# Kernel optimization log

Hardware: AMD Instinct MI355X
Metric: run time of the kernel (lower is better)

## Reference

```python
import jax, jax.numpy as jnp
import numpy as np

B = 4; C = 3; IMG = 256; P = 16; HP = 16; HW = 256
DIM = 512; DEPTH = 6; HEADS = 8; DH = 64
NS = 50; SH = 4; SDH = 64; ITERS = 3; RPD = 128; FF = 2048; N = NS + HW


def _ln(x, g, b):
    m = jnp.mean(x, -1, keepdims=True)
    v = jnp.var(x, -1, keepdims=True)
    return (x - m) * jax.lax.rsqrt(v + 1e-5) * g + b


def _rms(x, g):
    # lucidrains RMSNorm: F.normalize(x, dim=-1) * sqrt(dim) * gamma
    n = jnp.linalg.norm(x, axis=-1, keepdims=True)
    return x / jnp.maximum(n, 1e-12) * (DIM ** 0.5) * g


def setup_inputs() -> dict:
    key = jax.random.key(0)
    ks = iter(jax.random.split(key, 64))
    def W(*s):
        return jax.random.normal(next(ks), s, jnp.float32) * 0.02
    SI = SH * SDH
    d = {}
    d['images'] = jax.random.normal(next(ks), (B, C, IMG, IMG), jnp.float32)
    d['slot_noise'] = jax.random.normal(next(ks), (B, NS, DIM), jnp.float32)
    d['patch_w'] = W(C * P * P, DIM); d['patch_b'] = jnp.zeros((DIM,))
    d['hpos'] = W(HP, DIM); d['wpos'] = W(HP, DIM)
    d['rp_w1'] = W(2, RPD); d['rp_b1'] = jnp.zeros((RPD,))
    d['rp_w2'] = W(RPD, RPD); d['rp_b2'] = jnp.zeros((RPD,))
    d['rp_w3'] = W(RPD, HEADS); d['rp_b3'] = jnp.zeros((HEADS,))
    d['slots_mu'] = W(1, 1, DIM); d['slots_logsigma'] = jnp.zeros((1, 1, DIM))
    d['sa_ln_in_g'] = jnp.ones((DIM,)); d['sa_ln_in_b'] = jnp.zeros((DIM,))
    d['sa_ln_sl_g'] = jnp.ones((DIM,)); d['sa_ln_sl_b'] = jnp.zeros((DIM,))
    d['sa_wq'] = W(DIM, SI); d['sa_bq'] = jnp.zeros((SI,))
    d['sa_wk'] = W(DIM, SI); d['sa_bk'] = jnp.zeros((SI,))
    d['sa_wv'] = W(DIM, SI); d['sa_bv'] = jnp.zeros((SI,))
    d['sa_wo'] = W(SI, DIM); d['sa_bo'] = jnp.zeros((DIM,))
    d['gru_wih'] = W(DIM, 3 * DIM); d['gru_whh'] = W(DIM, 3 * DIM)
    d['gru_bih'] = jnp.zeros((3 * DIM,)); d['gru_bhh'] = jnp.zeros((3 * DIM,))
    d['sa_ln_ff_g'] = jnp.ones((DIM,)); d['sa_ln_ff_b'] = jnp.zeros((DIM,))
    d['sa_mlp_w1'] = W(DIM, DIM); d['sa_mlp_b1'] = jnp.zeros((DIM,))
    d['sa_mlp_w2'] = W(DIM, DIM); d['sa_mlp_b2'] = jnp.zeros((DIM,))
    d['s2c_w'] = W(DIM, 2); d['s2c_b'] = jnp.zeros((2,))
    d['attn_g'] = jnp.ones((DEPTH, DIM))
    d['wq'] = W(DEPTH, DIM, HEADS * DH); d['wk'] = W(DEPTH, DIM, HEADS * DH)
    d['wv'] = W(DEPTH, DIM, HEADS * DH); d['wo'] = W(DEPTH, HEADS * DH, DIM)
    d['ff_g'] = jnp.ones((DEPTH, DIM))
    d['ff_w1'] = W(DEPTH, DIM, FF); d['ff_b1'] = jnp.zeros((DEPTH, FF))
    d['ff_w2'] = W(DEPTH, FF, DIM); d['ff_b2'] = jnp.zeros((DEPTH, DIM))
    d['final_g'] = jnp.ones((DIM,))
    d['pred_w'] = W(DIM, DIM); d['pred_b'] = jnp.zeros((DIM,))
    return d


def reference(images, slot_noise, patch_w, patch_b, hpos, wpos,
              rp_w1, rp_b1, rp_w2, rp_b2, rp_w3, rp_b3,
              slots_mu, slots_logsigma, sa_ln_in_g, sa_ln_in_b, sa_ln_sl_g, sa_ln_sl_b,
              sa_wq, sa_bq, sa_wk, sa_bk, sa_wv, sa_bv, sa_wo, sa_bo,
              gru_wih, gru_whh, gru_bih, gru_bhh, sa_ln_ff_g, sa_ln_ff_b,
              sa_mlp_w1, sa_mlp_b1, sa_mlp_w2, sa_mlp_b2, s2c_w, s2c_b,
              attn_g, wq, wk, wv, wo, ff_g, ff_w1, ff_b1, ff_w2, ff_b2,
              final_g, pred_w, pred_b):
    b = images.shape[0]
    # patchify: b c (h p1) (w p2) -> b h w (p1 p2 c)
    x = images.reshape(b, C, HP, P, HP, P).transpose(0, 2, 4, 3, 5, 1).reshape(b, HP, HP, P * P * C)
    tokens = x @ patch_w + patch_b                     # [b, HP, HP, DIM]
    tokens = tokens + hpos[:, None, :] + wpos[None, :, :]
    tokens = tokens.reshape(b, HW, DIM)
    # --- multi-head slot attention ---
    inp = _ln(tokens, sa_ln_in_g, sa_ln_in_b)
    k = (inp @ sa_wk + sa_bk).reshape(b, HW, SH, SDH).transpose(0, 2, 1, 3)
    v = (inp @ sa_wv + sa_bv).reshape(b, HW, SH, SDH).transpose(0, 2, 1, 3)
    slots = slots_mu + jnp.exp(slots_logsigma) * slot_noise  # [b, NS, DIM]
    scale = SDH ** -0.5
    for _ in range(ITERS):
        prev = slots
        s = _ln(slots, sa_ln_sl_g, sa_ln_sl_b)
        q = (s @ sa_wq + sa_bq).reshape(b, NS, SH, SDH).transpose(0, 2, 1, 3)
        dots = jnp.einsum('bhid,bhjd->bhij', q, k) * scale     # [b, SH, NS, HW]
        attn = jax.nn.softmax(dots, axis=-2) + 1e-8            # softmax over slots
        attn = attn / jnp.sum(attn, -1, keepdims=True)         # weighted mean over inputs
        upd = jnp.einsum('bhij,bhjd->bhid', attn, v)
        upd = upd.transpose(0, 2, 1, 3).reshape(b, NS, SH * SDH) @ sa_wo + sa_bo
        # GRUCell(updates, prev_slots)
        gx = upd @ gru_wih + gru_bih
        gh = prev @ gru_whh + gru_bhh
        xr, xz, xn = jnp.split(gx, 3, -1)
        hr, hz, hn = jnp.split(gh, 3, -1)
        r = jax.nn.sigmoid(xr + hr)
        z = jax.nn.sigmoid(xz + hz)
        nn_ = jnp.tanh(xn + r * hn)
        slots = (1 - z) * nn_ + z * prev
        slots = slots + (jax.nn.relu(_ln(slots, sa_ln_ff_g, sa_ln_ff_b) @ sa_mlp_w1 + sa_mlp_b1) @ sa_mlp_w2 + sa_mlp_b2)
    objects = slots
    slot_coords = objects @ s2c_w + s2c_b              # [b, NS, 2]
    # --- relative position MLP bias (slots coords + patch grid) ---
    g = jnp.arange(HP, dtype=jnp.float32)
    grid = jnp.stack(jnp.meshgrid(g, g, indexing='ij'), -1).reshape(HW, 2)
    coords = jnp.concatenate([slot_coords, jnp.broadcast_to(grid, (b, HW, 2))], axis=1)  # [b, N, 2]
    rel = coords[:, :, None, :] - coords[:, None, :, :]   # [b, N, N, 2]
    hmid = jax.nn.silu(rel @ rp_w1 + rp_b1)
    hmid = jax.nn.silu(hmid @ rp_w2 + rp_b2)
    bias = jnp.transpose(hmid @ rp_w3 + rp_b3, (0, 3, 1, 2))  # [b, HEADS, N, N]
    # --- transformer with per-layer rel-pos bias ---
    x = jnp.concatenate([objects, tokens], axis=1)     # [b, N, DIM]
    ascale = DH ** -0.5
    for l in range(DEPTH):
        h = _rms(x, attn_g[l])
        qh = (h @ wq[l]).reshape(b, N, HEADS, DH).transpose(0, 2, 1, 3)
        kh = (h @ wk[l]).reshape(b, N, HEADS, DH).transpose(0, 2, 1, 3)
        vh = (h @ wv[l]).reshape(b, N, HEADS, DH).transpose(0, 2, 1, 3)
        sim = jnp.einsum('bhid,bhjd->bhij', qh, kh) * ascale + bias
        a = jax.nn.softmax(sim, -1)
        o = jnp.einsum('bhij,bhjd->bhid', a, vh).transpose(0, 2, 1, 3).reshape(b, N, HEADS * DH) @ wo[l]
        x = x + o
        h = _rms(x, ff_g[l])
        x = x + (jax.nn.gelu(h @ ff_w1[l] + ff_b1[l]) @ ff_w2[l] + ff_b2[l])
    x = _rms(x, final_g)
    return x[:, NS:] @ pred_w + pred_b                 # [b, HW, DIM]
```

## Files before the change

### kernel.cpp

```cpp
#include <hip/hip_runtime.h>
#include <hip/hip_bf16.h>

typedef __hip_bfloat16 bf16;
typedef short short8v __attribute__((ext_vector_type(8)));
typedef float float4v __attribute__((ext_vector_type(4)));

static __device__ __forceinline__ float b2f(bf16 x){ return __bfloat162float(x); }

static __device__ __forceinline__ float ldin(const void* p, size_t i, bool isbf) {
  return isbf ? b2f(((const bf16*)p)[i]) : ((const float*)p)[i];
}

static __device__ __forceinline__ unsigned short f2bu(float f) {
  bf16 h = __float2bfloat16(f);
  return *reinterpret_cast<unsigned short*>(&h);
}

#define CDIV(a,b) (((a)+(b)-1)/(b))

#define NB   4
#define NSL  50
#define HWT  256
#define NT   306
#define DIM  512
#define NH   8
#define FF   2048
#define RPP  28100
#define PCH  56200

static __device__ __forceinline__ void rp_decode(int q, int& i, int& j) {
  if (q < 15300) { i = q / NT; j = q % NT; }
  else { int r = q - 15300; i = NSL + r / NSL; j = r % NSL; }
}

__global__ void detect_k(const void* p, int* flag) {
  const unsigned short* u = (const unsigned short*)p;
  int t = threadIdx.x;
  int e = (u[t] >> 7) & 0xFF;
  __shared__ int anybad;
  if (t == 0) anybad = 0;
  __syncthreads();
  if (e >= 0x88) atomicOr(&anybad, 1);
  __syncthreads();
  if (t == 0) *flag = anybad ? 0 : 1;
}

struct WtArgs {
  const void* W[17];
  unsigned long long wto[17];
  int K[17], N[17];
  int base[18];
};

__global__ __launch_bounds__(256) void wtrans_all_k(WtArgs a, unsigned short* __restrict__ WT,
                                                    const int* __restrict__ flagp) {
  const bool isbf = *flagp != 0;
  int bid = blockIdx.x;
  int idx = 0;
#pragma unroll
  for (int i = 1; i < 17; ++i) if (bid >= a.base[i]) idx = i;
  int t0 = bid - a.base[idx];
  const int K = a.K[idx], N = a.N[idx];
  const int tilesN = N >> 6;
  const int perLayer = tilesN * (K >> 6);
  const int layer = t0 / perLayer, rem = t0 % perLayer;
  const int n0 = (rem % tilesN) * 64, k0 = (rem / tilesN) * 64;
  const void* W = a.W[idx];
  unsigned short* dst0 = WT + a.wto[idx];
  const size_t slice = (size_t)K * N * layer;

  __shared__ unsigned short S[64 * 72];
  int t = threadIdx.x;
  int kk = t >> 4, nn = (t & 15) * 4;
#pragma unroll
  for (int r = 0; r < 4; ++r) {
    int k = k0 + kk + r * 16;
    unsigned short v[4];
    if (isbf) {
      ushort4 u = *(const ushort4*)((const unsigned short*)W + slice + (size_t)k * N + n0 + nn);
      v[0]=u.x; v[1]=u.y; v[2]=u.z; v[3]=u.w;
    } else {
      float4 f = *(const float4*)((const float*)W + slice + (size_t)k * N + n0 + nn);
      v[0]=f2bu(f.x); v[1]=f2bu(f.y); v[2]=f2bu(f.z); v[3]=f2bu(f.w);
    }
#pragma unroll
    for (int i = 0; i < 4; ++i) S[(nn + i) * 72 + kk + r * 16] = v[i];
  }
  __syncthreads();
  int nr = t >> 2, kc = (t & 3) * 16;
  short8v s0 = *(const short8v*)&S[nr * 72 + kc];
  short8v s1 = *(const short8v*)&S[nr * 72 + kc + 8];
  unsigned short* dst = dst0 + slice + (size_t)(n0 + nr) * K + k0 + kc;
  *(short8v*)dst = s0;
  *(short8v*)(dst + 8) = s1;
}

#define LDK 72
static __device__ __forceinline__ void gemm_body2(
    const void* __restrict__ A, int aty,
    const unsigned short* __restrict__ WT,
    const void* __restrict__ bias, size_t boff,
    void* __restrict__ C, int oty,
    int M, int N, int K, int kbeg, int kend,
    int act, int mode, bool isbf)
{
  __shared__ unsigned short As[64 * LDK];
  __shared__ unsigned short Bs[64 * LDK];
  const int tid = threadIdx.x;
  const int lane = tid & 63, wave = tid >> 6;
  const int quad = lane >> 4, ti = lane & 15;
  const int wm = (wave & 1) * 32, wn = (wave >> 1) * 32;
  const int bm = blockIdx.y * 64, bn = blockIdx.x * 64;
  const int srow = tid >> 2, sch = (tid & 3) * 16;

  unsigned short ha[16], hb[16];
  const int gm = bm + srow;
  const bool aok = gm < M;
  const unsigned short* Abf = (const unsigned short*)A + (size_t)gm * K;
  const float*          Af  = (const float*)A + (size_t)gm * K;
  const unsigned short* Bp  = WT + (size_t)(bn + srow) * K;

  auto fetchA = [&](int k0) {
    if (aok) {
      if (aty) {
        const ushort4* ap = (const ushort4*)(Abf + k0 + sch);
#pragma unroll
        for (int i = 0; i < 4; ++i) {
          ushort4 u = ap[i];
          ha[i*4+0]=u.x; ha[i*4+1]=u.y; ha[i*4+2]=u.z; ha[i*4+3]=u.w;
        }
      } else {
        const float4* ap = (const float4*)(Af + k0 + sch);
#pragma unroll
        for (int i = 0; i < 4; ++i) {
          float4 f = ap[i];
          ha[i*4+0]=f2bu(f.x); ha[i*4+1]=f2bu(f.y); ha[i*4+2]=f2bu(f.z); ha[i*4+3]=f2bu(f.w);
        }
      }
    } else {
#pragma unroll
      for (int i = 0; i < 16; ++i) ha[i] = 0;
    }
  };
  auto fetchB = [&](int k0) {
    const ushort4* bp = (const ushort4*)(Bp + k0 + sch);
#pragma unroll
    for (int i = 0; i < 4; ++i) {
      ushort4 u = bp[i];
      hb[i*4+0]=u.x; hb[i*4+1]=u.y; hb[i*4+2]=u.z; hb[i*4+3]=u.w;
    }
  };

  float4v acc00 = {0,0,0,0}, acc01 = {0,0,0,0}, acc10 = {0,0,0,0}, acc11 = {0,0,0,0};
  fetchA(kbeg); fetchB(kbeg);
  for (int k0 = kbeg; k0 < kend; k0 += 64) {
    *(short8v*)&As[srow * LDK + sch]     = *(short8v*)ha;
    *(short8v*)&As[srow * LDK + sch + 8] = *(short8v*)(ha + 8);
    *(short8v*)&Bs[srow * LDK + sch]     = *(short8v*)hb;
    *(short8v*)&Bs[srow * LDK + sch + 8] = *(short8v*)(hb + 8);
    __syncthreads();
    if (k0 + 64 < kend) { fetchA(k0 + 64); fetchB(k0 + 64); }
#pragma unroll
    for (int ks = 0; ks < 2; ++ks) {
      short8v a0 = *reinterpret_cast<const short8v*>(&As[(wm + ti)      * LDK + ks * 32 + quad * 8]);
      short8v a1 = *reinterpret_cast<const short8v*>(&As[(wm + 16 + ti) * LDK + ks * 32 + quad * 8]);
      short8v b0 = *reinterpret_cast<const short8v*>(&Bs[(wn + ti)      * LDK + ks * 32 + quad * 8]);
      short8v b1 = *reinterpret_cast<const short8v*>(&Bs[(wn + 16 + ti) * LDK + ks * 32 + quad * 8]);
      acc00 = __builtin_amdgcn_mfma_f32_16x16x32_bf16(a0, b0, acc00, 0, 0, 0);
      acc01 = __builtin_amdgcn_mfma_f32_16x16x32_bf16(a0, b1, acc01, 0, 0, 0);
      acc10 = __builtin_amdgcn_mfma_f32_16x16x32_bf16(a1, b0, acc10, 0, 0, 0);
      acc11 = __builtin_amdgcn_mfma_f32_16x16x32_bf16(a1, b1, acc11, 0, 0, 0);
    }
    __syncthreads();
  }

  float4v accs[2][2] = {{acc00, acc01}, {acc10, acc11}};
#pragma unroll
  for (int mi = 0; mi < 2; ++mi) {
#pragma unroll
    for (int ni = 0; ni < 2; ++ni) {
      int row0 = bm + wm + mi * 16 + quad * 4;
      int col  = bn + wn + ni * 16 + ti;
      float bv = (bias && kbeg == 0) ? ldin(bias, boff + col, isbf) : 0.f;
#pragma unroll
      for (int r = 0; r < 4; ++r) {
        int row = row0 + r;
        if (row >= M) continue;
        float v = accs[mi][ni][r] + bv;
        if (act == 1) v = fmaxf(v, 0.f);
        else if (act == 2) {
          float u = 0.7978845608028654f * (v + 0.044715f * v * v * v);
          v = 0.5f * v * (1.f + tanhf(u));
        } else if (act == 3) {
          v = v / (1.f + expf(-v));
        }
        size_t idx = (size_t)row * N + col;
        if (oty) ((bf16*)C)[idx] = __float2bfloat16(v);
        else {
          float* Cf = (float*)C;
          if (mode == 2) atomicAdd(&Cf[idx], v);
          else if (mode == 1) Cf[idx] += v;
          else Cf[idx] = v;
        }
      }
    }
  }
}

__global__ __launch_bounds__(256) void gemm_mfma(
    const void* A, int aty, const unsigned short* WT, size_t woff,
    const void* bias, size_t boff, void* C, int oty,
    int M, int N, int K, int act, int accum, int zsplit, const int* __restrict__ flagp)
{
  int ksz = K / zsplit;
  int kbeg = blockIdx.z * ksz;
  int mode = zsplit > 1 ? 2 : (accum ? 1 : 0);
  gemm_body2(A, aty, WT + woff, bias, boff, C, oty, M, N, K, kbeg, kbeg + ksz,
             act, mode, *flagp != 0);
}

__global__ __launch_bounds__(256) void gemm_mfma_tri(
    const void* A, int aty, const unsigned short* WT, size_t o0, size_t o1, size_t o2,
    void* C0, void* C1, void* C2, int oty, int M, int N, int K,
    const int* __restrict__ flagp)
{
  size_t o = blockIdx.z == 0 ? o0 : (blockIdx.z == 1 ? o1 : o2);
  void* C = blockIdx.z == 0 ? C0 : (blockIdx.z == 1 ? C1 : C2);
  gemm_body2(A, aty, WT + o, nullptr, 0, C, oty, M, N, K, 0, K, 0, 0, *flagp != 0);
}

__global__ __launch_bounds__(256) void gemm_mfma_duo(
    const void* A0, const void* A1, int aty, const unsigned short* WT, size_t o0, size_t o1,
    const void* bias0, const void* bias1, void* C0, void* C1, int oty,
    int M, int N, int K, const int* __restrict__ flagp)
{
  const void* A = blockIdx.z ? A1 : A0;
  size_t o = blockIdx.z ? o1 : o0;
  const void* bias = blockIdx.z ? bias1 : bias0;
  void* C = blockIdx.z ? C1 : C0;
  gemm_body2(A, aty, WT + o, bias, 0, C, oty, M, N, K, 0, K, 0, 0, *flagp != 0);
}

__global__ void s2c_k(const float* __restrict__ slots, const void* __restrict__ w,
                      const void* __restrict__ bv, float* __restrict__ sc,
                      const int* __restrict__ flagp) {
  const bool isbf = *flagp != 0;
  int row = blockIdx.x, t = threadIdx.x;
  const float* x = slots + (size_t)row * DIM;
  float v0 = x[t], v1 = x[t + 256];
  float a0 = v0 * ldin(w, 2 * t, isbf)     + v1 * ldin(w, 2 * (t + 256), isbf);
  float a1 = v0 * ldin(w, 2 * t + 1, isbf) + v1 * ldin(w, 2 * (t + 256) + 1, isbf);
  __shared__ float r0[256], r1[256];
  r0[t] = a0; r1[t] = a1;
  __syncthreads();
  for (int o = 128; o > 0; o >>= 1) {
    if (t < o) { r0[t] += r0[t + o]; r1[t] += r1[t + o]; }
    __syncthreads();
  }
  if (t == 0) {
    sc[row * 2]     = r0[0] + ldin(bv, 0, isbf);
    sc[row * 2 + 1] = r1[0] + ldin(bv, 1, isbf);
  }
}

__global__ void patchify_k(const void* __restrict__ img, unsigned short* __restrict__ xp,
                           const int* __restrict__ flagp) {
  const bool isbf = *flagp != 0;
  int i = blockIdx.x * 256 + threadIdx.x;
  if (i >= NB * HWT * 768) return;
  int col = i % 768, row = i / 768;
  int c = col % 3, p2 = (col / 3) & 15, p1 = col / 48;
  int w = row & 15, h = (row >> 4) & 15, b = row >> 8;
  xp[i] = f2bu(ldin(img, (((size_t)(b * 3 + c) * 256 + h * 16 + p1) * 256) + w * 16 + p2, isbf));
}

__global__ void addpos_k(float* __restrict__ tok, const void* __restrict__ hp,
                         const void* __restrict__ wp, const int* __restrict__ flagp) {
  const bool isbf = *flagp != 0;
  int i = blockIdx.x * 256 + threadIdx.x;
  if (i >= NB * HWT * DIM) return;
  int d = i & 511;
  int row = i >> 9;
  int w = row & 15, h = (row >> 4) & 15;
  tok[i] += ldin(hp, h * DIM + d, isbf) + ldin(wp, w * DIM + d, isbf);
}

__global__ void ln512_k(const float* __restrict__ X, const void* __restrict__ g,
                        const void* __restrict__ b, unsigned short* __restrict__ Y,
                        const int* __restrict__ flagp) {
  const bool isbf = *flagp != 0;
  int row = blockIdx.x, t = threadIdx.x;
  const float* x = X + (size_t)row * DIM;
  float v0 = x[t], v1 = x[t + 256];
  __shared__ float rs[256], rq[256];
  rs[t] = v0 + v1; rq[t] = v0 * v0 + v1 * v1;
  __syncthreads();
  for (int o = 128; o > 0; o >>= 1) {
    if (t < o) { rs[t] += rs[t + o]; rq[t] += rq[t + o]; }
    __syncthreads();
  }
  float mean = rs[0] * (1.f / 512.f);
  float var  = rq[0] * (1.f / 512.f) - mean * mean;
  float inv  = rsqrtf(var + 1e-5f);
  unsigned short* y = Y + (size_t)row * DIM;
  y[t]       = f2bu((v0 - mean) * inv * ldin(g, t, isbf)       + ldin(b, t, isbf));
  y[t + 256] = f2bu((v1 - mean) * inv * ldin(g, t + 256, isbf) + ldin(b, t + 256, isbf));
}

__global__ void rms512_k(const float* __restrict__ X, const void* __restrict__ g,
                         int goff, unsigned short* __restrict__ Y, const int* __restrict__ flagp) {
  const bool isbf = *flagp != 0;
  int row = blockIdx.x, t = threadIdx.x;
  const float* x = X + (size_t)row * DIM;
  float v0 = x[t], v1 = x[t + 256];
  __shared__ float rq[256];
  rq[t] = v0 * v0 + v1 * v1;
  __syncthreads();
  for (int o = 128; o > 0; o >>= 1) {
    if (t < o) rq[t] += rq[t + o];
    __syncthreads();
  }
  float nrm = sqrtf(rq[0]);
  float sc = 22.62741699796952f / fmaxf(nrm, 1e-12f);
  unsigned short* y = Y + (size_t)row * DIM;
  y[t]       = f2bu(v0 * sc * ldin(g, goff + t, isbf));
  y[t + 256] = f2bu(v1 * sc * ldin(g, goff + t + 256, isbf));
}

__global__ void slots_init_k(const void* __restrict__ mu, const void* __restrict__ ls,
                             const void* __restrict__ noise, float* __restrict__ slots,
                             const int* __restrict__ flagp) {
  const bool isbf = *flagp != 0;
  int i = blockIdx.x * 256 + threadIdx.x;
  if (i >= NB * NSL * DIM) return;
  int d = i & 511;
  slots[i] = ldin(mu, d, isbf) + expf(ldin(ls, d, isbf)) * ldin(noise, i, isbf);
}

__global__ void slot_dots_k(const float* __restrict__ q, const float* __restrict__ k,
                            float* __restrict__ dots) {
  int blk = blockIdx.x;
  int i = blk % 50, h = (blk / 50) & 3, b = blk / 200;
  int j = threadIdx.x;
  __shared__ float qs[64];
  if (threadIdx.x < 64) qs[threadIdx.x] = q[((size_t)(b * 50 + i)) * 256 + h * 64 + threadIdx.x];
  __syncthreads();
  const float* kr = k + ((size_t)(b * 256 + j)) * 256 + h * 64;
  float s = 0.f;
#pragma unroll 8
  for (int d = 0; d < 64; ++d) s = fmaf(qs[d], kr[d], s);
  dots[(((size_t)(b * 4 + h) * 50) + i) * 256 + j] = s * 0.125f;
}

__global__ void softmax_slots_k(float* __restrict__ dots) {
  int idx = blockIdx.x * 256 + threadIdx.x;
  if (idx >= 4096) return;
  int j = idx & 255, h = (idx >> 8) & 3, b = idx >> 10;
  float* base = dots + ((size_t)(b * 4 + h) * 50) * 256 + j;
  float m = -1e30f;
  for (int i = 0; i < 50; ++i) m = fmaxf(m, base[i * 256]);
  float s = 0.f;
  for (int i = 0; i < 50; ++i) { float e = expf(base[i * 256] - m); base[i * 256] = e; s += e; }
  float inv = 1.f / s;
  for (int i = 0; i < 50; ++i) base[i * 256] *= inv;
}

__global__ void renorm_attn_k(float* __restrict__ attn) {
  int t = threadIdx.x;
  float* row = attn + (size_t)blockIdx.x * 256;
  float v = row[t] + 1e-8f;
  __shared__ float rs[256];
  rs[t] = v;
  __syncthreads();
  for (int o = 128; o > 0; o >>= 1) {
    if (t < o) rs[t] += rs[t + o];
    __syncthreads();
  }
  row[t] = v / rs[0];
}

__global__ void slot_upd_k(const float* __restrict__ attn, const float* __restrict__ v,
                           float* __restrict__ upd) {
  int bi = blockIdx.x;
  int b = bi / 50, i = bi % 50;
  int t = threadIdx.x, h = t >> 6;
  const float* arow = attn + ((size_t)((b * 4 + h) * 50) + i) * 256;
  float s = 0.f;
  for (int j = 0; j < 256; ++j) s = fmaf(arow[j], v[((size_t)(b * 256 + j)) * 256 + t], s);
  upd[(size_t)bi * 256 + t] = s;
}

__global__ void gru_k(const float* __restrict__ gx, const float* __restrict__ gh,
                      float* __restrict__ slots) {
  int i = blockIdx.x * 256 + threadIdx.x;
  if (i >= NB * NSL * DIM) return;
  int row = i >> 9, d = i & 511;
  size_t b3 = (size_t)row * 1536;
  float xr = gx[b3 + d], xz = gx[b3 + 512 + d], xn = gx[b3 + 1024 + d];
  float hr = gh[b3 + d], hz = gh[b3 + 512 + d], hn = gh[b3 + 1024 + d];
  float r = 1.f / (1.f + expf(-(xr + hr)));
  float z = 1.f / (1.f + expf(-(xz + hz)));
  float n = tanhf(xn + r * hn);
  float prev = slots[i];
  slots[i] = (1.f - z) * n + z * prev;
}

__global__ void build_coords_k(const float* __restrict__ sc, float* __restrict__ coords) {
  int i = blockIdx.x * 256 + threadIdx.x;
  if (i >= NB * NT) return;
  int b = i / NT, n = i % NT;
  float cx, cy;
  if (n < NSL) { cx = sc[(b * NSL + n) * 2]; cy = sc[(b * NSL + n) * 2 + 1]; }
  else { int t = n - NSL; cx = (float)(t >> 4); cy = (float)(t & 15); }
  coords[i * 2] = cx; coords[i * 2 + 1] = cy;
}

__global__ void relpos_table_k(const void* w1, const void* b1, const void* w2,
                               const void* b2, const void* w3, const void* b3,
                               float* __restrict__ tab, const int* __restrict__ flagp) {
  const bool isbf = *flagp != 0;
  int blk = blockIdx.x;
  float r0 = (float)(blk / 31 - 15), r1 = (float)(blk % 31 - 15);
  int t = threadIdx.x;
  __shared__ float h1[128], h2[128];
  float a = fmaf(r0, ldin(w1, t, isbf), fmaf(r1, ldin(w1, 128 + t, isbf), ldin(b1, t, isbf)));
  h1[t] = a / (1.f + expf(-a));
  __syncthreads();
  float s = ldin(b2, t, isbf);
#pragma unroll 4
  for (int k = 0; k < 128; ++k) s = fmaf(h1[k], ldin(w2, k * 128 + t, isbf), s);
  h2[t] = s / (1.f + expf(-s));
  __syncthreads();
  if (t < 8) {
    float o = ldin(b3, t, isbf);
#pragma unroll 4
    for (int k = 0; k < 128; ++k) o = fmaf(h2[k], ldin(w3, k * 8 + t, isbf), o);
    tab[blk * 8 + t] = o;
  }
}

__global__ void bias_fill_k(const float* __restrict__ tab, float* __restrict__ bias) {
  int i = blockIdx.x * 256 + threadIdx.x;
  if (i >= NB * NH * HWT * HWT) return;
  int jj = i & 255, ii = (i >> 8) & 255, h = (i >> 16) & 7, b = i >> 19;
  int di = (ii >> 4) - (jj >> 4) + 15;
  int dj = (ii & 15) - (jj & 15) + 15;
  bias[(((size_t)(b * NH + h) * NT) + NSL + ii) * NT + NSL + jj] = tab[(di * 31 + dj) * 8 + h];
}

__global__ void rp_l1_k(const float* __restrict__ coords, const void* w1, const void* b1,
                        unsigned short* __restrict__ H, int pbase, int pcount,
                        const int* __restrict__ flagp) {
  const bool isbf = *flagp != 0;
  int idx = blockIdx.x * 256 + threadIdx.x;
  if (idx >= pcount * 128) return;
  int pl = idx >> 7, u = idx & 127;
  int p = pbase + pl;
  int q = p % RPP, bb = p / RPP;
  int ii, jj;
  rp_decode(q, ii, jj);
  float r0 = coords[(bb * NT + ii) * 2]     - coords[(bb * NT + jj) * 2];
  float r1 = coords[(bb * NT + ii) * 2 + 1] - coords[(bb * NT + jj) * 2 + 1];
  float a = fmaf(r0, ldin(w1, u, isbf), fmaf(r1, ldin(w1, 128 + u, isbf), ldin(b1, u, isbf)));
  H[(size_t)pl * 128 + u] = f2bu(a / (1.f + expf(-a)));
}

__global__ __launch_bounds__(256) void rp_l3_k(
    const unsigned short* __restrict__ H2, const void* w3, const void* b3,
    float* __restrict__ bias, int pbase, int pcount, const int* __restrict__ flagp) {
  const bool isbf = *flagp != 0;
  __shared__ float W3s[128 * 8];
  int t = threadIdx.x;
  for (int e = t; e < 1024; e += 256) W3s[e] = ldin(w3, e, isbf);
  __syncthreads();
  int pl = blockIdx.x * 32 + (t >> 3), hh = t & 7;
  if (pl >= pcount) return;
  int p = pbase + pl;
  int q = p % RPP, bb = p / RPP;
  int ii, jj;
  rp_decode(q, ii, jj);
  float s = ldin(b3, hh, isbf);
  const unsigned short* hrow = H2 + (size_t)pl * 128;
#pragma unroll 8
  for (int k = 0; k < 128; ++k) {
    bf16 hv = *reinterpret_cast<const bf16*>(&hrow[k]);
    s = fmaf(b2f(hv), W3s[k * 8 + hh], s);
  }
  bias[((size_t)(bb * NH + hh) * NT + ii) * NT + jj] = s;
}

__global__ void build_x_k(const float* __restrict__ slots, const float* __restrict__ tok,
                          float* __restrict__ x) {
  int i = blockIdx.x * 256 + threadIdx.x;
  if (i >= NB * NT * DIM) return;
  int d = i & 511, n = (i >> 9) % NT, b = i / (NT * DIM);
  x[i] = (n < NSL) ? slots[((size_t)(b * NSL + n)) * DIM + d]
                   : tok[((size_t)(b * HWT + (n - NSL))) * DIM + d];
}

__global__ __launch_bounds__(256) void attn_fused_k(
    const unsigned short* __restrict__ Qb, const unsigned short* __restrict__ Kb,
    const unsigned short* __restrict__ Vb, const float* __restrict__ bias,
    unsigned short* __restrict__ Ob)
{
  const int bh = blockIdx.y, b = bh >> 3, h = bh & 7;
  const int i0 = blockIdx.x * 32;
  __shared__ unsigned short Qs[32 * 72];
  __shared__ unsigned short Ks[64 * 72];
  __shared__ float S[32 * 332];
  unsigned short* P = (unsigned short*)S;

  const int tid = threadIdx.x;
  const int lane = tid & 63, wave = tid >> 6, quad = lane >> 4, ti = lane & 15;
  const int mi = wave & 1, nh = wave >> 1;

  {
    int r = tid >> 3, c = (tid & 7) * 8;
    int gi = i0 + r;
    ushort4 u0 = {0,0,0,0}, u1 = {0,0,0,0};
    if (gi < NT) {
      const ushort4* p = (const ushort4*)(Qb + ((size_t)(b * NT + gi)) * DIM + h * 64 + c);
      u0 = p[0]; u1 = p[1];
    }
    *(ushort4*)&Qs[r * 72 + c] = u0;
    *(ushort4*)&Qs[r * 72 + c + 4] = u1;
  }

  for (int kt = 0; kt < 5; ++kt) {
    __syncthreads();
    {
      int kr = tid >> 2, c = (tid & 3) * 16;
      int gj = kt * 64 + kr;
      ushort4 v[4] = {{0,0,0,0},{0,0,0,0},{0,0,0,0},{0,0,0,0}};
      if (gj < NT) {
        const ushort4* p = (const ushort4*)(Kb + ((size_t)(b * NT + gj)) * DIM + h * 64 + c);
#pragma unroll
        for (int i = 0; i < 4; ++i) v[i] = p[i];
      }
#pragma unroll
      for (int i = 0; i < 4; ++i) *(ushort4*)&Ks[kr * 72 + c + i * 4] = v[i];
    }
    __syncthreads();
#pragma unroll
    for (int ntl = 0; ntl < 2; ++ntl) {
      int nt = nh * 2 + ntl;
      float4v acc = {0,0,0,0};
#pragma unroll
      for (int ks = 0; ks < 2; ++ks) {
        short8v a  = *(const short8v*)&Qs[(mi * 16 + ti) * 72 + ks * 32 + quad * 8];
        short8v bb = *(const short8v*)&Ks[(nt * 16 + ti) * 72 + ks * 32 + quad * 8];
        acc = __builtin_amdgcn_mfma_f32_16x16x32_bf16(a, bb, acc, 0, 0, 0);
      }
      int colL = kt * 64 + nt * 16 + ti;
      int row0 = mi * 16 + quad * 4;
#pragma unroll
      for (int r = 0; r < 4; ++r) {
        int row_g = i0 + row0 + r;
        float val;
        if (colL < NT) {
          float bv = (row_g < NT) ? bias[((size_t)bh * NT + row_g) * NT + colL] : 0.f;
          val = acc[r] * 0.125f + bv;
        } else val = -1e30f;
        S[(row0 + r) * 332 + colL] = val;
      }
    }
  }
  __syncthreads();

  {
    int rl = tid >> 3, sub = tid & 7;
    float sv[40];
#pragma unroll
    for (int k = 0; k < 40; ++k) sv[k] = S[rl * 332 + sub + k * 8];
    float m = -1e30f;
#pragma unroll
    for (int k = 0; k < 40; ++k) m = fmaxf(m, sv[k]);
    m = fmaxf(m, __shfl_xor(m, 1));
    m = fmaxf(m, __shfl_xor(m, 2));
    m = fmaxf(m, __shfl_xor(m, 4));
    float s = 0.f;
#pragma unroll
    for (int k = 0; k < 40; ++k) { float e = __expf(sv[k] - m); sv[k] = e; s += e; }
    s += __shfl_xor(s, 1);
    s += __shfl_xor(s, 2);
    s += __shfl_xor(s, 4);
    float inv = 1.f / s;
    __syncthreads();
#pragma unroll
    for (int k = 0; k < 40; ++k) P[rl * 664 + sub + k * 8] = f2bu(sv[k] * inv);
  }

  float4v oacc[2] = {{0,0,0,0},{0,0,0,0}};
  for (int vt = 0; vt < 5; ++vt) {
    __syncthreads();
    {
      int key = tid & 63, d0 = (tid >> 6) * 16;
      int gj = vt * 64 + key;
      unsigned short hv[16];
      if (gj < NT) {
        const ushort4* p = (const ushort4*)(Vb + ((size_t)(b * NT + gj)) * DIM + h * 64 + d0);
#pragma unroll
        for (int i = 0; i < 4; ++i) {
          ushort4 u = p[i];
          hv[i*4+0]=u.x; hv[i*4+1]=u.y; hv[i*4+2]=u.z; hv[i*4+3]=u.w;
        }
      } else {
#pragma unroll
        for (int i = 0; i < 16; ++i) hv[i] = 0;
      }
#pragma unroll
      for (int i = 0; i < 16; ++i) Ks[(d0 + i) * 72 + key] = hv[i];
    }
    __syncthreads();
#pragma unroll
    for (int ntl = 0; ntl < 2; ++ntl) {
      int nt = nh * 2 + ntl;
#pragma unroll
      for (int ks = 0; ks < 2; ++ks) {
        short8v a  = *(const short8v*)&P[(mi * 16 + ti) * 664 + vt * 64 + ks * 32 + quad * 8];
        short8v bb = *(const short8v*)&Ks[(nt * 16 + ti) * 72 + ks * 32 + quad * 8];
        oacc[ntl] = __builtin_amdgcn_mfma_f32_16x16x32_bf16(a, bb, oacc[ntl], 0, 0, 0);
      }
    }
  }

#pragma unroll
  for (int ntl = 0; ntl < 2; ++ntl) {
    int dim = nh * 32 + ntl * 16 + ti;
#pragma unroll
    for (int r = 0; r < 4; ++r) {
      int row_g = i0 + mi * 16 + quad * 4 + r;
      if (row_g < NT)
        Ob[((size_t)(b * NT + row_g)) * DIM + h * 64 + dim] = f2bu(oacc[ntl][r]);
    }
  }
}

__global__ void write_out_k(const float* __restrict__ tmp, void* __restrict__ out,
                            const int* __restrict__ flagp) {
  const bool isbf = *flagp != 0;
  int i = blockIdx.x * 256 + threadIdx.x;
  if (i >= NB * HWT * DIM) return;
  int d = i & 511, tt = (i >> 9) & 255, b = i / (HWT * DIM);
  float v = tmp[((size_t)(b * NT + NSL + tt)) * DIM + d];
  if (isbf) ((bf16*)out)[i] = __float2bfloat16(v);
  else      ((float*)out)[i] = v;
}

extern "C" void kernel_launch(void* const* d_in, const int* in_sizes, int n_in,
                              void* d_out, int out_size, void* d_ws, size_t ws_size,
                              hipStream_t stream) {
  const void* images        = d_in[0];
  const void* slot_noise    = d_in[1];
  const void* patch_w       = d_in[2];
  const void* patch_b       = d_in[3];
  const void* hpos          = d_in[4];
  const void* wpos          = d_in[5];
  const void* rp_w1         = d_in[6];
  const void* rp_b1         = d_in[7];
  const void* rp_w2         = d_in[8];
  const void* rp_b2         = d_in[9];
  const void* rp_w3         = d_in[10];
  const void* rp_b3         = d_in[11];
  const void* slots_mu      = d_in[12];
  const void* slots_logsig  = d_in[13];
  const void* sa_ln_in_g    = d_in[14];
  const void* sa_ln_in_b    = d_in[15];
  const void* sa_ln_sl_g    = d_in[16];
  const void* sa_ln_sl_b    = d_in[17];
  const void* sa_wq         = d_in[18];
  const void* sa_bq         = d_in[19];
  const void* sa_wk         = d_in[20];
  const void* sa_bk         = d_in[21];
  const void* sa_wv         = d_in[22];
  const void* sa_bv         = d_in[23];
  const void* sa_wo         = d_in[24];
  const void* sa_bo         = d_in[25];
  const void* gru_wih       = d_in[26];
  const void* gru_whh       = d_in[27];
  const void* gru_bih       = d_in[28];
  const void* gru_bhh       = d_in[29];
  const void* sa_ln_ff_g    = d_in[30];
  const void* sa_ln_ff_b    = d_in[31];
  const void* sa_mlp_w1     = d_in[32];
  const void* sa_mlp_b1     = d_in[33];
  const void* sa_mlp_w2     = d_in[34];
  const void* sa_mlp_b2     = d_in[35];
  const void* s2c_w         = d_in[36];
  const void* s2c_b         = d_in[37];
  const void* attn_g        = d_in[38];
  const void* wq            = d_in[39];
  const void* wk            = d_in[40];
  const void* wv            = d_in[41];
  const void* wo            = d_in[42];
  const void* ff_g          = d_in[43];
  const void* ff_w1         = d_in[44];
  const void* ff_b1         = d_in[45];
  const void* ff_w2         = d_in[46];
  const void* ff_b2         = d_in[47];
  const void* final_g       = d_in[48];
  const void* pred_w        = d_in[49];
  const void* pred_b        = d_in[50];

  float* ws = (float*)d_ws;
  int* FLAG = (int*)ws;
  size_t off = 16;
  auto alloc = [&](size_t n) { float* p = ws + off; off += (n + 15) & ~(size_t)15; return p; };
  float* TOK   = alloc((size_t)NB * HWT * DIM);
  unsigned short* INPB = (unsigned short*)alloc((size_t)NB * HWT * DIM / 2);
  float* KB    = alloc((size_t)NB * HWT * 256);
  float* VB    = alloc((size_t)NB * HWT * 256);
  float* SLOTS = alloc((size_t)NB * NSL * DIM);
  unsigned short* SLNB = (unsigned short*)alloc((size_t)NB * NSL * DIM / 2);
  float* QB    = alloc((size_t)NB * NSL * 256);
  float* ATT   = alloc((size_t)NB * 4 * NSL * HWT);
  float* UPD   = alloc((size_t)NB * NSL * 256);
  float* UPDP  = alloc((size_t)NB * NSL * DIM);
  unsigned short* HIDSB = (unsigned short*)alloc((size_t)NB * NSL * DIM / 2);
  float* SC    = alloc((size_t)NB * NSL * 2);
  float* CRD   = alloc((size_t)NB * NT * 2);
  float* TAB   = alloc((size_t)961 * 8);
  float* BIAS  = alloc((size_t)NB * NH * NT * NT);
  float* X     = alloc((size_t)NB * NT * DIM);
  unsigned short* HBB  = (unsigned short*)alloc((size_t)NB * NT * DIM / 2);
  unsigned short* QHB  = (unsigned short*)alloc((size_t)NB * NT * DIM / 2);
  unsigned short* KHB  = (unsigned short*)alloc((size_t)NB * NT * DIM / 2);
  unsigned short* VHB  = (unsigned short*)alloc((size_t)NB * NT * DIM / 2);
  float* SIM   = alloc((size_t)NB * NH * NT * NT);
  unsigned short* OBB  = (unsigned short*)alloc((size_t)NB * NT * DIM / 2);
  unsigned short* FFHB = (unsigned short*)alloc((size_t)NB * NT * FF / 2);
  float* OUTT  = alloc((size_t)NB * NT * DIM);
  unsigned short* XPB = (unsigned short*)OUTT;
  float* GX = SIM;
  float* GH = SIM + (size_t)NB * NSL * 1536;
  const size_t oPatch = 0;
  const size_t oKw    = oPatch + (size_t)512 * 768;
  const size_t oVw    = oKw    + (size_t)256 * 512;
  const size_t oQw    = oVw    + (size_t)256 * 512;
  const size_t oWo    = oQw    + (size_t)256 * 512;
  const size_t oGih   = oWo    + (size_t)512 * 256;
  const size_t oGhh   = oGih   + (size_t)1536 * 512;
  const size_t oMlp1  = oGhh   + (size_t)1536 * 512;
  const size_t oMlp2  = oMlp1  + (size_t)512 * 512;
  const size_t oRp2   = oMlp2  + (size_t)512 * 512;
  const size_t oWq    = oRp2   + (size_t)128 * 128;
  const size_t oWk    = oWq    + (size_t)6 * 512 * 512;
  const size_t oWv    = oWk    + (size_t)6 * 512 * 512;
  const size_t oWol   = oWv    + (size_t)6 * 512 * 512;
  const size_t oFf1   = oWol   + (size_t)6 * 512 * 512;
  const size_t oFf2   = oFf1   + (size_t)6 * 512 * 2048;
  const size_t oPred  = oFf2   + (size_t)6 * 2048 * 512;
  const size_t wtTotal = oPred + (size_t)512 * 512;
  unsigned short* WTS = (unsigned short*)alloc((wtTotal + 1) / 2);
  (void)ws_size; (void)in_sizes; (void)n_in; (void)out_size;

#define GEMMM(A_, ATY_, WOFF_, BIAS_, BOFF_, C_, OTY_, M_, N_, K_, ACT_, ACC_, ZS_) \
  gemm_mfma<<<dim3((N_)/64, CDIV((M_),64), (ZS_)), 256, 0, stream>>>( \
      A_, ATY_, WTS, (size_t)(WOFF_), BIAS_, (size_t)(BOFF_), C_, OTY_, M_, N_, K_, ACT_, ACC_, ZS_, FLAG)

  const int MROW = NB * NT;
  const int MS   = NB * NSL;

  detect_k<<<1, 256, 0, stream>>>(images, FLAG);
  {
    WtArgs a;
    const void* Wp[17] = { patch_w, sa_wk, sa_wv, sa_wq, sa_wo, gru_wih, gru_whh,
                           sa_mlp_w1, sa_mlp_w2, rp_w2, wq, wk, wv, wo, ff_w1, ff_w2, pred_w };
    const size_t Oo[17] = { oPatch, oKw, oVw, oQw, oWo, oGih, oGhh,
                            oMlp1, oMlp2, oRp2, oWq, oWk, oWv, oWol, oFf1, oFf2, oPred };
    const int Kk[17] = {768,512,512,512,256,512,512,512,512,128,512,512,512,512,512,2048,512};
    const int Nn[17] = {512,256,256,256,512,1536,1536,512,512,128,512,512,512,512,2048,512,512};
    const int Ll[17] = {1,1,1,1,1,1,1,1,1,1,6,6,6,6,6,6,1};
    int acc = 0;
    for (int i = 0; i < 17; ++i) {
      a.W[i] = Wp[i]; a.wto[i] = Oo[i]; a.K[i] = Kk[i]; a.N[i] = Nn[i];
      a.base[i] = acc;
      acc += Ll[i] * (Kk[i] >> 6) * (Nn[i] >> 6);
    }
    a.base[17] = acc;
    wtrans_all_k<<<acc, 256, 0, stream>>>(a, WTS, FLAG);
  }

  patchify_k<<<CDIV(NB*HWT*768, 256), 256, 0, stream>>>(images, XPB, FLAG);
  hipMemsetAsync(TOK, 0, (size_t)NB * HWT * DIM * sizeof(float), stream);
  GEMMM(XPB, 1, oPatch, patch_b, 0, TOK, 0, NB*HWT, DIM, 768, 0, 0, 3);
  addpos_k<<<CDIV(NB*HWT*DIM, 256), 256, 0, stream>>>(TOK, hpos, wpos, FLAG);

  ln512_k<<<NB*HWT, 256, 0, stream>>>(TOK, sa_ln_in_g, sa_ln_in_b, INPB, FLAG);
  gemm_mfma_duo<<<dim3(4, 16, 2), 256, 0, stream>>>(
      INPB, INPB, 1, WTS, oKw, oVw, sa_bk, sa_bv, KB, VB, 0, NB*HWT, 256, DIM, FLAG);
  slots_init_k<<<CDIV(NB*NSL*DIM, 256), 256, 0, stream>>>(slots_mu, slots_logsig, slot_noise, SLOTS, FLAG);

  for (int it = 0; it < 3; ++it) {
    ln512_k<<<MS, 256, 0, stream>>>(SLOTS, sa_ln_sl_g, sa_ln_sl_b, SLNB, FLAG);
    GEMMM(SLNB, 1, oQw, sa_bq, 0, QB, 0, MS, 256, DIM, 0, 0, 1);
    slot_dots_k<<<NB*4*NSL, 256, 0, stream>>>(QB, KB, ATT);
    softmax_slots_k<<<16, 256, 0, stream>>>(ATT);
    renorm_attn_k<<<NB*4*NSL, 256, 0, stream>>>(ATT);
    slot_upd_k<<<MS, 256, 0, stream>>>(ATT, VB, UPD);
    GEMMM(UPD, 0, oWo, sa_bo, 0, UPDP, 0, MS, DIM, 256, 0, 0, 1);
    gemm_mfma_duo<<<dim3(24, 4, 2), 256, 0, stream>>>(
        UPDP, SLOTS, 0, WTS, oGih, oGhh, gru_bih, gru_bhh, GX, GH, 0, MS, 1536, DIM, FLAG);
    gru_k<<<CDIV(NB*NSL*DIM, 256), 256, 0, stream>>>(GX, GH, SLOTS);
    ln512_k<<<MS, 256, 0, stream>>>(SLOTS, sa_ln_ff_g, sa_ln_ff_b, SLNB, FLAG);
    GEMMM(SLNB, 1, oMlp1, sa_mlp_b1, 0, HIDSB, 1, MS, DIM, DIM, 1, 0, 1);
    GEMMM(HIDSB, 1, oMlp2, sa_mlp_b2, 0, SLOTS, 0, MS, DIM, DIM, 0, 1, 1);
  }

  s2c_k<<<MS, 256, 0, stream>>>(SLOTS, s2c_w, s2c_b, SC, FLAG);
  build_coords_k<<<CDIV(NB*NT, 256), 256, 0, stream>>>(SC, CRD);
  relpos_table_k<<<961, 128, 0, stream>>>(rp_w1, rp_b1, rp_w2, rp_b2, rp_w3, rp_b3, TAB, FLAG);
  bias_fill_k<<<CDIV(NB*NH*HWT*HWT, 256), 256, 0, stream>>>(TAB, BIAS);
  {
    unsigned short* H1 = HBB;
    unsigned short* H2 = HBB + (size_t)PCH * 128;
    for (int c = 0; c < 2; ++c) {
      int pb = c * PCH;
      rp_l1_k<<<CDIV(PCH*128, 256), 256, 0, stream>>>(CRD, rp_w1, rp_b1, H1, pb, PCH, FLAG);
      GEMMM(H1, 1, oRp2, rp_b2, 0, H2, 1, PCH, 128, 128, 3, 0, 1);
      rp_l3_k<<<CDIV(PCH,32), 256, 0, stream>>>(H2, rp_w3, rp_b3, BIAS, pb, PCH, FLAG);
    }
  }

  build_x_k<<<CDIV(NB*NT*DIM, 256), 256, 0, stream>>>(SLOTS, TOK, X);
  for (int l = 0; l < 6; ++l) {
    size_t lw = (size_t)l * 512 * 512;
    rms512_k<<<MROW, 256, 0, stream>>>(X, attn_g, l * DIM, HBB, FLAG);
    gemm_mfma_tri<<<dim3(8, 20, 3), 256, 0, stream>>>(
        HBB, 1, WTS, oWq + lw, oWk + lw, oWv + lw, QHB, KHB, VHB, 1, MROW, DIM, DIM, FLAG);
    attn_fused_k<<<dim3(10, NB*NH), 256, 0, stream>>>(QHB, KHB, VHB, BIAS, OBB);
    GEMMM(OBB, 1, oWol + lw, (const void*)nullptr, 0, X, 0, MROW, DIM, DIM, 0, 1, 2);
    rms512_k<<<MROW, 256, 0, stream>>>(X, ff_g, l * DIM, HBB, FLAG);
    GEMMM(HBB, 1, oFf1 + (size_t)l * 512 * 2048, ff_b1, l * FF, FFHB, 1, MROW, FF, DIM, 2, 0, 1);
    GEMMM(FFHB, 1, oFf2 + (size_t)l * 2048 * 512, ff_b2, l * DIM, X, 0, MROW, DIM, FF, 0, 1, 4);
  }

  rms512_k<<<MROW, 256, 0, stream>>>(X, final_g, 0, HBB, FLAG);
  hipMemsetAsync(OUTT, 0, (size_t)NB * NT * DIM * sizeof(float), stream);
  GEMMM(HBB, 1, oPred, pred_b, 0, OUTT, 0, MROW, DIM, DIM, 0, 0, 2);
  write_out_k<<<CDIV(NB*HWT*DIM, 256), 256, 0, stream>>>(OUTT, d_out, FLAG);

#undef GEMMM
}
```

Measured before the change: 1.173 ms.

## Fuse norms into GEMM prologues and relpos MLP into one kernel

LayerNorm and RMSNorm are folded into the A-operand load of the following GEMM: each block computes per-row statistics itself, which removes the separate norm kernels and their bf16 intermediate buffers. The positional add and the output slicing move into the GEMM epilogue, and split-K is dropped for the patch and prediction GEMMs. The three-stage relative-position MLP becomes one kernel that keeps its hidden activations in LDS, and the slot softmax and renormalisation are merged into one kernel. In exchange, every GEMM block re-reads full fp32 rows for the statistics, which is redundant across column blocks, and some GEMMs lose split-K parallelism.

```diff
diff --git a/kernel.cpp b/kernel.cpp
--- a/kernel.cpp
+++ b/kernel.cpp
@@ -26,7 +26,6 @@
 #define NH   8
 #define FF   2048
 #define RPP  28100
-#define PCH  56200
 
 static __device__ __forceinline__ void rp_decode(int q, int& i, int& j) {
   if (q < 15300) { i = q / NT; j = q % NT; }
@@ -96,16 +95,21 @@
 }
 
 #define LDK 72
-static __device__ __forceinline__ void gemm_body2(
+static __device__ __forceinline__ void gemm_body3(
     const void* __restrict__ A, int aty,
+    int nrm, const void* __restrict__ ng, const void* __restrict__ nbv, int ngoff,
     const unsigned short* __restrict__ WT,
     const void* __restrict__ bias, size_t boff,
     void* __restrict__ C, int oty,
     int M, int N, int K, int kbeg, int kend,
-    int act, int mode, bool isbf)
+    int act, int mode, int spec,
+    const void* __restrict__ p0, const void* __restrict__ p1,
+    bool isbf)
 {
   __shared__ unsigned short As[64 * LDK];
   __shared__ unsigned short Bs[64 * LDK];
+  __shared__ float NPm[64], NPs[64];
+  __shared__ float RS[256], RQ[256];
   const int tid = threadIdx.x;
   const int lane = tid & 63, wave = tid >> 6;
   const int quad = lane >> 4, ti = lane & 15;
@@ -113,12 +117,44 @@
   const int bm = blockIdx.y * 64, bn = blockIdx.x * 64;
   const int srow = tid >> 2, sch = (tid & 3) * 16;
 
-  unsigned short ha[16], hb[16];
   const int gm = bm + srow;
   const bool aok = gm < M;
+
+  if (nrm) {
+    int r = tid >> 2, qd = tid & 3;
+    float s = 0.f, q = 0.f;
+    if (bm + r < M) {
+      const float4* xp = (const float4*)((const float*)A + (size_t)(bm + r) * K + qd * 128);
+#pragma unroll
+      for (int i = 0; i < 32; ++i) {
+        float4 f = xp[i];
+        s += f.x + f.y + f.z + f.w;
+        q += f.x*f.x + f.y*f.y + f.z*f.z + f.w*f.w;
+      }
+    }
+    RS[tid] = s; RQ[tid] = q;
+    __syncthreads();
+    if (qd == 0) {
+      float ss = RS[tid] + RS[tid+1] + RS[tid+2] + RS[tid+3];
+      float qq = RQ[tid] + RQ[tid+1] + RQ[tid+2] + RQ[tid+3];
+      if (nrm == 1) {
+        float mean = ss * (1.f / 512.f);
+        float var  = qq * (1.f / 512.f) - mean * mean;
+        NPm[r] = mean; NPs[r] = rsqrtf(var + 1e-5f);
+      } else {
+        NPm[r] = 0.f;
+        NPs[r] = 22.62741699796952f / fmaxf(sqrtf(qq), 1e-12f);
+      }
+    }
+    __syncthreads();
+  }
+
+  unsigned short ha[16], hb[16];
   const unsigned short* Abf = (const unsigned short*)A + (size_t)gm * K;
   const float*          Af  = (const float*)A + (size_t)gm * K;
   const unsigned short* Bp  = WT + (size_t)(bn + srow) * K;
+  const float nmean = nrm ? NPm[srow] : 0.f;
+  const float nscl  = nrm ? NPs[srow] : 0.f;
 
   auto fetchA = [&](int k0) {
     if (aok) {
@@ -128,6 +164,28 @@
         for (int i = 0; i < 4; ++i) {
           ushort4 u = ap[i];
           ha[i*4+0]=u.x; ha[i*4+1]=u.y; ha[i*4+2]=u.z; ha[i*4+3]=u.w;
+        }
+      } else if (nrm == 1) {
+        const float4* ap = (const float4*)(Af + k0 + sch);
+#pragma unroll
+        for (int i = 0; i < 4; ++i) {
+          float4 f = ap[i];
+          int kk = ngoff + k0 + sch + i * 4;
+          ha[i*4+0]=f2bu((f.x-nmean)*nscl*ldin(ng,kk+0,isbf)+ldin(nbv,kk+0,isbf));
+          ha[i*4+1]=f2bu((f.y-nmean)*nscl*ldin(ng,kk+1,isbf)+ldin(nbv,kk+1,isbf));
+          ha[i*4+2]=f2bu((f.z-nmean)*nscl*ldin(ng,kk+2,isbf)+ldin(nbv,kk+2,isbf));
+          ha[i*4+3]=f2bu((f.w-nmean)*nscl*ldin(ng,kk+3,isbf)+ldin(nbv,kk+3,isbf));
+        }
+      } else if (nrm == 2) {
+        const float4* ap = (const float4*)(Af + k0 + sch);
+#pragma unroll
+        for (int i = 0; i < 4; ++i) {
+          float4 f = ap[i];
+          int kk = ngoff + k0 + sch + i * 4;
+          ha[i*4+0]=f2bu(f.x*nscl*ldin(ng,kk+0,isbf));
+          ha[i*4+1]=f2bu(f.y*nscl*ldin(ng,kk+1,isbf));
+          ha[i*4+2]=f2bu(f.z*nscl*ldin(ng,kk+2,isbf));
+          ha[i*4+3]=f2bu(f.w*nscl*ldin(ng,kk+3,isbf));
         }
       } else {
         const float4* ap = (const float4*)(Af + k0 + sch);
@@ -194,43 +252,61 @@
         } else if (act == 3) {
           v = v / (1.f + expf(-v));
         }
-        size_t idx = (size_t)row * N + col;
-        if (oty) ((bf16*)C)[idx] = __float2bfloat16(v);
-        else {
-          float* Cf = (float*)C;
-          if (mode == 2) atomicAdd(&Cf[idx], v);
-          else if (mode == 1) Cf[idx] += v;
-          else Cf[idx] = v;
+        if (spec == 2) {
+          int hh = (row >> 4) & 15, ww = row & 15;
+          v += ldin(p0, hh * N + col, isbf) + ldin(p1, ww * N + col, isbf);
         }
+        if (spec == 1) {
+          int b_ = row / NT, n_ = row % NT;
+          if (n_ >= NSL) {
+            size_t oi = ((size_t)(b_ * HWT + (n_ - NSL))) * N + col;
+            if (isbf) ((bf16*)C)[oi] = __float2bfloat16(v);
+            else      ((float*)C)[oi] = v;
+          }
+        } else {
+          size_t idx = (size_t)row * N + col;
+          if (oty) ((bf16*)C)[idx] = __float2bfloat16(v);
+          else {
+            float* Cf = (float*)C;
+            if (mode == 2) atomicAdd(&Cf[idx], v);
+            else if (mode == 1) Cf[idx] += v;
+            else Cf[idx] = v;
+          }
+        }
       }
     }
   }
 }
 
 __global__ __launch_bounds__(256) void gemm_mfma(
-    const void* A, int aty, const unsigned short* WT, size_t woff,
+    const void* A, int aty, int nrm, const void* ng, const void* nbv, int ngoff,
+    const unsigned short* WT, size_t woff,
     const void* bias, size_t boff, void* C, int oty,
-    int M, int N, int K, int act, int accum, int zsplit, const int* __restrict__ flagp)
+    int M, int N, int K, int act, int accum, int zsplit,
+    int spec, const void* p0, const void* p1, const int* __restrict__ flagp)
 {
   int ksz = K / zsplit;
   int kbeg = blockIdx.z * ksz;
   int mode = zsplit > 1 ? 2 : (accum ? 1 : 0);
-  gemm_body2(A, aty, WT + woff, bias, boff, C, oty, M, N, K, kbeg, kbeg + ksz,
-             act, mode, *flagp != 0);
+  gemm_body3(A, aty, nrm, ng, nbv, ngoff, WT + woff, bias, boff, C, oty,
+             M, N, K, kbeg, kbeg + ksz, act, mode, spec, p0, p1, *flagp != 0);
 }
 
 __global__ __launch_bounds__(256) void gemm_mfma_tri(
-    const void* A, int aty, const unsigned short* WT, size_t o0, size_t o1, size_t o2,
+    const void* A, int aty, int nrm, const void* ng, int ngoff,
+    const unsigned short* WT, size_t o0, size_t o1, size_t o2,
     void* C0, void* C1, void* C2, int oty, int M, int N, int K,
     const int* __restrict__ flagp)
 {
   size_t o = blockIdx.z == 0 ? o0 : (blockIdx.z == 1 ? o1 : o2);
   void* C = blockIdx.z == 0 ? C0 : (blockIdx.z == 1 ? C1 : C2);
-  gemm_body2(A, aty, WT + o, nullptr, 0, C, oty, M, N, K, 0, K, 0, 0, *flagp != 0);
+  gemm_body3(A, aty, nrm, ng, nullptr, ngoff, WT + o, nullptr, 0, C, oty,
+             M, N, K, 0, K, 0, 0, 0, nullptr, nullptr, *flagp != 0);
 }
 
 __global__ __launch_bounds__(256) void gemm_mfma_duo(
-    const void* A0, const void* A1, int aty, const unsigned short* WT, size_t o0, size_t o1,
+    const void* A0, const void* A1, int aty, int nrm, const void* ng, const void* nbv,
+    const unsigned short* WT, size_t o0, size_t o1,
     const void* bias0, const void* bias1, void* C0, void* C1, int oty,
     int M, int N, int K, const int* __restrict__ flagp)
 {
@@ -238,7 +314,115 @@
   size_t o = blockIdx.z ? o1 : o0;
   const void* bias = blockIdx.z ? bias1 : bias0;
   void* C = blockIdx.z ? C1 : C0;
-  gemm_body2(A, aty, WT + o, bias, 0, C, oty, M, N, K, 0, K, 0, 0, *flagp != 0);
+  gemm_body3(A, aty, nrm, ng, nbv, 0, WT + o, bias, 0, C, oty,
+             M, N, K, 0, K, 0, 0, 0, nullptr, nullptr, *flagp != 0);
+}
+
+__global__ __launch_bounds__(256) void gemm_rp_k(
+    const float* __restrict__ CRD_, const void* w1, const void* b1,
+    const unsigned short* __restrict__ WT, size_t woff,
+    const void* b2, const void* w3, const void* b3,
+    float* __restrict__ bias, const int* __restrict__ flagp)
+{
+  const bool isbf = *flagp != 0;
+  const int NPAIR = NB * RPP;
+  __shared__ unsigned short As[64 * 136];
+  __shared__ unsigned short Bs[128 * 136];
+  __shared__ float W3s[1024];
+  const int tid = threadIdx.x;
+  const int bm = blockIdx.x * 64;
+
+  for (int e = tid; e < 1024; e += 256) W3s[e] = ldin(w3, e, isbf);
+  {
+    const unsigned short* Bp = WT + woff;
+    int nrow = tid >> 1, half = (tid & 1) * 64;
+    const short8v* src = (const short8v*)(Bp + (size_t)nrow * 128 + half);
+#pragma unroll
+    for (int i = 0; i < 8; ++i)
+      *(short8v*)&Bs[nrow * 136 + half + i * 8] = src[i];
+  }
+  {
+    int r = tid >> 2, k0 = (tid & 3) * 32;
+    int p = bm + r;
+    float r0 = 0.f, r1 = 0.f;
+    bool ok = p < NPAIR;
+    if (ok) {
+      int q = p % RPP, bb = p / RPP;
+      int ii, jj; rp_decode(q, ii, jj);
+      r0 = CRD_[(bb * NT + ii) * 2]     - CRD_[(bb * NT + jj) * 2];
+      r1 = CRD_[(bb * NT + ii) * 2 + 1] - CRD_[(bb * NT + jj) * 2 + 1];
+    }
+    for (int k = 0; k < 32; ++k) {
+      int kk = k0 + k;
+      float a = fmaf(r0, ldin(w1, kk, isbf), fmaf(r1, ldin(w1, 128 + kk, isbf), ldin(b1, kk, isbf)));
+      a = a / (1.f + expf(-a));
+      As[r * 136 + kk] = ok ? f2bu(a) : (unsigned short)0;
+    }
+  }
+  __syncthreads();
+
+  const int lane = tid & 63, wave = tid >> 6, quad = lane >> 4, ti = lane & 15;
+  const int wm = (wave & 1) * 32, wn = (wave >> 1) * 32;
+  float4v acc[2][2][2];
+#pragma unroll
+  for (int nb2 = 0; nb2 < 2; ++nb2)
+#pragma unroll
+    for (int mi = 0; mi < 2; ++mi)
+#pragma unroll
+      for (int ni = 0; ni < 2; ++ni) acc[nb2][mi][ni] = (float4v){0,0,0,0};
+
+#pragma unroll
+  for (int ks = 0; ks < 4; ++ks) {
+    short8v a0 = *(const short8v*)&As[(wm + ti)      * 136 + ks * 32 + quad * 8];
+    short8v a1 = *(const short8v*)&As[(wm + 16 + ti) * 136 + ks * 32 + quad * 8];
+#pragma unroll
+    for (int nb2 = 0; nb2 < 2; ++nb2) {
+      short8v b0v = *(const short8v*)&Bs[(nb2 * 64 + wn + ti)      * 136 + ks * 32 + quad * 8];
+      short8v b1v = *(const short8v*)&Bs[(nb2 * 64 + wn + 16 + ti) * 136 + ks * 32 + quad * 8];
+      acc[nb2][0][0] = __builtin_amdgcn_mfma_f32_16x16x32_bf16(a0, b0v, acc[nb2][0][0], 0, 0, 0);
+      acc[nb2][0][1] = __builtin_amdgcn_mfma_f32_16x16x32_bf16(a0, b1v, acc[nb2][0][1], 0, 0, 0);
+      acc[nb2][1][0] = __builtin_amdgcn_mfma_f32_16x16x32_bf16(a1, b0v, acc[nb2][1][0], 0, 0, 0);
+      acc[nb2][1][1] = __builtin_amdgcn_mfma_f32_16x16x32_bf16(a1, b1v, acc[nb2][1][1], 0, 0, 0);
+    }
+  }
+  __syncthreads();
+
+  unsigned short* Hs = As;
+#pragma unroll
+  for (int nb2 = 0; nb2 < 2; ++nb2)
+#pragma unroll
+    for (int mi = 0; mi < 2; ++mi)
+#pragma unroll
+      for (int ni = 0; ni < 2; ++ni) {
+        int row0 = wm + mi * 16 + quad * 4;
+        int col  = nb2 * 64 + wn + ni * 16 + ti;
+        float bv = ldin(b2, col, isbf);
+#pragma unroll
+        for (int r = 0; r < 4; ++r) {
+          float v = acc[nb2][mi][ni][r] + bv;
+          v = v / (1.f + expf(-v));
+          Hs[(row0 + r) * 136 + col] = f2bu(v);
+        }
+      }
+  __syncthreads();
+
+#pragma unroll
+  for (int s = 0; s < 2; ++s) {
+    int item = tid + s * 256;
+    int r = item >> 3, hh = item & 7;
+    int p = bm + r;
+    if (p < NPAIR) {
+      int q = p % RPP, bb = p / RPP;
+      int ii, jj; rp_decode(q, ii, jj);
+      float acc3 = ldin(b3, hh, isbf);
+#pragma unroll 8
+      for (int k = 0; k < 128; ++k) {
+        bf16 hv = *reinterpret_cast<const bf16*>(&Hs[r * 136 + k]);
+        acc3 = fmaf(b2f(hv), W3s[k * 8 + hh], acc3);
+      }
+      bias[((size_t)(bb * NH + hh) * NT + ii) * NT + jj] = acc3;
+    }
+  }
 }
 
 __global__ void s2c_k(const float* __restrict__ slots, const void* __restrict__ w,
@@ -274,59 +458,6 @@
   xp[i] = f2bu(ldin(img, (((size_t)(b * 3 + c) * 256 + h * 16 + p1) * 256) + w * 16 + p2, isbf));
 }
 
-__global__ void addpos_k(float* __restrict__ tok, const void* __restrict__ hp,
-                         const void* __restrict__ wp, const int* __restrict__ flagp) {
-  const bool isbf = *flagp != 0;
-  int i = blockIdx.x * 256 + threadIdx.x;
-  if (i >= NB * HWT * DIM) return;
-  int d = i & 511;
-  int row = i >> 9;
-  int w = row & 15, h = (row >> 4) & 15;
-  tok[i] += ldin(hp, h * DIM + d, isbf) + ldin(wp, w * DIM + d, isbf);
-}
-
-__global__ void ln512_k(const float* __restrict__ X, const void* __restrict__ g,
-                        const void* __restrict__ b, unsigned short* __restrict__ Y,
-                        const int* __restrict__ flagp) {
-  const bool isbf = *flagp != 0;
-  int row = blockIdx.x, t = threadIdx.x;
-  const float* x = X + (size_t)row * DIM;
-  float v0 = x[t], v1 = x[t + 256];
-  __shared__ float rs[256], rq[256];
-  rs[t] = v0 + v1; rq[t] = v0 * v0 + v1 * v1;
-  __syncthreads();
-  for (int o = 128; o > 0; o >>= 1) {
-    if (t < o) { rs[t] += rs[t + o]; rq[t] += rq[t + o]; }
-    __syncthreads();
-  }
-  float mean = rs[0] * (1.f / 512.f);
-  float var  = rq[0] * (1.f / 512.f) - mean * mean;
-  float inv  = rsqrtf(var + 1e-5f);
-  unsigned short* y = Y + (size_t)row * DIM;
-  y[t]       = f2bu((v0 - mean) * inv * ldin(g, t, isbf)       + ldin(b, t, isbf));
-  y[t + 256] = f2bu((v1 - mean) * inv * ldin(g, t + 256, isbf) + ldin(b, t + 256, isbf));
-}
-
-__global__ void rms512_k(const float* __restrict__ X, const void* __restrict__ g,
-                         int goff, unsigned short* __restrict__ Y, const int* __restrict__ flagp) {
-  const bool isbf = *flagp != 0;
-  int row = blockIdx.x, t = threadIdx.x;
-  const float* x = X + (size_t)row * DIM;
-  float v0 = x[t], v1 = x[t + 256];
-  __shared__ float rq[256];
-  rq[t] = v0 * v0 + v1 * v1;
-  __syncthreads();
-  for (int o = 128; o > 0; o >>= 1) {
-    if (t < o) rq[t] += rq[t + o];
-    __syncthreads();
-  }
-  float nrm = sqrtf(rq[0]);
-  float sc = 22.62741699796952f / fmaxf(nrm, 1e-12f);
-  unsigned short* y = Y + (size_t)row * DIM;
-  y[t]       = f2bu(v0 * sc * ldin(g, goff + t, isbf));
-  y[t + 256] = f2bu(v1 * sc * ldin(g, goff + t + 256, isbf));
-}
-
 __global__ void slots_init_k(const void* __restrict__ mu, const void* __restrict__ ls,
                              const void* __restrict__ noise, float* __restrict__ slots,
                              const int* __restrict__ flagp) {
@@ -352,31 +483,36 @@
   dots[(((size_t)(b * 4 + h) * 50) + i) * 256 + j] = s * 0.125f;
 }
 
-__global__ void softmax_slots_k(float* __restrict__ dots) {
-  int idx = blockIdx.x * 256 + threadIdx.x;
-  if (idx >= 4096) return;
-  int j = idx & 255, h = (idx >> 8) & 3, b = idx >> 10;
-  float* base = dots + ((size_t)(b * 4 + h) * 50) * 256 + j;
+__global__ __launch_bounds__(256) void sm_renorm_k(float* __restrict__ att) {
+  __shared__ float S[NSL * 257];
+  const int t = threadIdx.x;
+  float* base = att + (size_t)blockIdx.x * (NSL * HWT);
+  float v[NSL];
+#pragma unroll
+  for (int i = 0; i < NSL; ++i) v[i] = base[i * HWT + t];
   float m = -1e30f;
-  for (int i = 0; i < 50; ++i) m = fmaxf(m, base[i * 256]);
+#pragma unroll
+  for (int i = 0; i < NSL; ++i) m = fmaxf(m, v[i]);
   float s = 0.f;
-  for (int i = 0; i < 50; ++i) { float e = expf(base[i * 256] - m); base[i * 256] = e; s += e; }
+#pragma unroll
+  for (int i = 0; i < NSL; ++i) { float e = expf(v[i] - m); v[i] = e; s += e; }
   float inv = 1.f / s;
-  for (int i = 0; i < 50; ++i) base[i * 256] *= inv;
-}
-
-__global__ void renorm_attn_k(float* __restrict__ attn) {
-  int t = threadIdx.x;
-  float* row = attn + (size_t)blockIdx.x * 256;
-  float v = row[t] + 1e-8f;
-  __shared__ float rs[256];
-  rs[t] = v;
-  __syncthreads();
-  for (int o = 128; o > 0; o >>= 1) {
-    if (t < o) rs[t] += rs[t + o];
-    __syncthreads();
-  }
-  row[t] = v / rs[0];
+#pragma unroll
+  for (int i = 0; i < NSL; ++i) S[i * 257 + t] = fmaf(v[i], inv, 1e-8f);
+  __syncthreads();
+  const int w = t >> 6, l = t & 63;
+  for (int r = w; r < NSL; r += 4) {
+    float a0 = S[r * 257 + l],        a1 = S[r * 257 + 64 + l];
+    float a2 = S[r * 257 + 128 + l],  a3 = S[r * 257 + 192 + l];
+    float s4 = a0 + a1 + a2 + a3;
+#pragma unroll
+    for (int o = 1; o < 64; o <<= 1) s4 += __shfl_xor(s4, o);
+    float inv2 = 1.f / s4;
+    base[r * HWT + l]       = a0 * inv2;
+    base[r * HWT + 64 + l]  = a1 * inv2;
+    base[r * HWT + 128 + l] = a2 * inv2;
+    base[r * HWT + 192 + l] = a3 * inv2;
+  }
 }
 
 __global__ void slot_upd_k(const float* __restrict__ attn, const float* __restrict__ v,
@@ -448,47 +584,6 @@
   bias[(((size_t)(b * NH + h) * NT) + NSL + ii) * NT + NSL + jj] = tab[(di * 31 + dj) * 8 + h];
 }
 
-__global__ void rp_l1_k(const float* __restrict__ coords, const void* w1, const void* b1,
-                        unsigned short* __restrict__ H, int pbase, int pcount,
-                        const int* __restrict__ flagp) {
-  const bool isbf = *flagp != 0;
-  int idx = blockIdx.x * 256 + threadIdx.x;
-  if (idx >= pcount * 128) return;
-  int pl = idx >> 7, u = idx & 127;
-  int p = pbase + pl;
-  int q = p % RPP, bb = p / RPP;
-  int ii, jj;
-  rp_decode(q, ii, jj);
-  float r0 = coords[(bb * NT + ii) * 2]     - coords[(bb * NT + jj) * 2];
-  float r1 = coords[(bb * NT + ii) * 2 + 1] - coords[(bb * NT + jj) * 2 + 1];
-  float a = fmaf(r0, ldin(w1, u, isbf), fmaf(r1, ldin(w1, 128 + u, isbf), ldin(b1, u, isbf)));
-  H[(size_t)pl * 128 + u] = f2bu(a / (1.f + expf(-a)));
-}
-
-__global__ __launch_bounds__(256) void rp_l3_k(
-    const unsigned short* __restrict__ H2, const void* w3, const void* b3,
-    float* __restrict__ bias, int pbase, int pcount, const int* __restrict__ flagp) {
-  const bool isbf = *flagp != 0;
-  __shared__ float W3s[128 * 8];
-  int t = threadIdx.x;
-  for (int e = t; e < 1024; e += 256) W3s[e] = ldin(w3, e, isbf);
-  __syncthreads();
-  int pl = blockIdx.x * 32 + (t >> 3), hh = t & 7;
-  if (pl >= pcount) return;
-  int p = pbase + pl;
-  int q = p % RPP, bb = p / RPP;
-  int ii, jj;
-  rp_decode(q, ii, jj);
-  float s = ldin(b3, hh, isbf);
-  const unsigned short* hrow = H2 + (size_t)pl * 128;
-#pragma unroll 8
-  for (int k = 0; k < 128; ++k) {
-    bf16 hv = *reinterpret_cast<const bf16*>(&hrow[k]);
-    s = fmaf(b2f(hv), W3s[k * 8 + hh], s);
-  }
-  bias[((size_t)(bb * NH + hh) * NT + ii) * NT + jj] = s;
-}
-
 __global__ void build_x_k(const float* __restrict__ slots, const float* __restrict__ tok,
                           float* __restrict__ x) {
   int i = blockIdx.x * 256 + threadIdx.x;
@@ -634,17 +729,6 @@
         Ob[((size_t)(b * NT + row_g)) * DIM + h * 64 + dim] = f2bu(oacc[ntl][r]);
     }
   }
-}
-
-__global__ void write_out_k(const float* __restrict__ tmp, void* __restrict__ out,
-                            const int* __restrict__ flagp) {
-  const bool isbf = *flagp != 0;
-  int i = blockIdx.x * 256 + threadIdx.x;
-  if (i >= NB * HWT * DIM) return;
-  int d = i & 511, tt = (i >> 9) & 255, b = i / (HWT * DIM);
-  float v = tmp[((size_t)(b * NT + NSL + tt)) * DIM + d];
-  if (isbf) ((bf16*)out)[i] = __float2bfloat16(v);
-  else      ((float*)out)[i] = v;
 }
 
 extern "C" void kernel_launch(void* const* d_in, const int* in_sizes, int n_in,
@@ -733,6 +817,7 @@
   unsigned short* XPB = (unsigned short*)OUTT;
   float* GX = SIM;
   float* GH = SIM + (size_t)NB * NSL * 1536;
+  (void)INPB; (void)SLNB; (void)HBB;
   const size_t oPatch = 0;
   const size_t oKw    = oPatch + (size_t)512 * 768;
   const size_t oVw    = oKw    + (size_t)256 * 512;
@@ -754,10 +839,6 @@
   unsigned short* WTS = (unsigned short*)alloc((wtTotal + 1) / 2);
   (void)ws_size; (void)in_sizes; (void)n_in; (void)out_size;
 
-#define GEMMM(A_, ATY_, WOFF_, BIAS_, BOFF_, C_, OTY_, M_, N_, K_, ACT_, ACC_, ZS_) \
-  gemm_mfma<<<dim3((N_)/64, CDIV((M_),64), (ZS_)), 256, 0, stream>>>( \
-      A_, ATY_, WTS, (size_t)(WOFF_), BIAS_, (size_t)(BOFF_), C_, OTY_, M_, N_, K_, ACT_, ACC_, ZS_, FLAG)
-
   const int MROW = NB * NT;
   const int MS   = NB * NSL;
 
@@ -782,63 +863,63 @@
   }
 
   patchify_k<<<CDIV(NB*HWT*768, 256), 256, 0, stream>>>(images, XPB, FLAG);
-  hipMemsetAsync(TOK, 0, (size_t)NB * HWT * DIM * sizeof(float), stream);
-  GEMMM(XPB, 1, oPatch, patch_b, 0, TOK, 0, NB*HWT, DIM, 768, 0, 0, 3);
-  addpos_k<<<CDIV(NB*HWT*DIM, 256), 256, 0, stream>>>(TOK, hpos, wpos, FLAG);
-
-  ln512_k<<<NB*HWT, 256, 0, stream>>>(TOK, sa_ln_in_g, sa_ln_in_b, INPB, FLAG);
+  gemm_mfma<<<dim3(8, 16, 1), 256, 0, stream>>>(
+      XPB, 1, 0, nullptr, nullptr, 0, WTS, oPatch, patch_b, 0, TOK, 0,
+      NB*HWT, DIM, 768, 0, 0, 1, 2, hpos, wpos, FLAG);
+
   gemm_mfma_duo<<<dim3(4, 16, 2), 256, 0, stream>>>(
-      INPB, INPB, 1, WTS, oKw, oVw, sa_bk, sa_bv, KB, VB, 0, NB*HWT, 256, DIM, FLAG);
+      TOK, TOK, 0, 1, sa_ln_in_g, sa_ln_in_b,
+      WTS, oKw, oVw, sa_bk, sa_bv, KB, VB, 0, NB*HWT, 256, DIM, FLAG);
   slots_init_k<<<CDIV(NB*NSL*DIM, 256), 256, 0, stream>>>(slots_mu, slots_logsig, slot_noise, SLOTS, FLAG);
 
   for (int it = 0; it < 3; ++it) {
-    ln512_k<<<MS, 256, 0, stream>>>(SLOTS, sa_ln_sl_g, sa_ln_sl_b, SLNB, FLAG);
-    GEMMM(SLNB, 1, oQw, sa_bq, 0, QB, 0, MS, 256, DIM, 0, 0, 1);
+    gemm_mfma<<<dim3(4, 4, 1), 256, 0, stream>>>(
+        SLOTS, 0, 1, sa_ln_sl_g, sa_ln_sl_b, 0, WTS, oQw, sa_bq, 0, QB, 0,
+        MS, 256, DIM, 0, 0, 1, 0, nullptr, nullptr, FLAG);
     slot_dots_k<<<NB*4*NSL, 256, 0, stream>>>(QB, KB, ATT);
-    softmax_slots_k<<<16, 256, 0, stream>>>(ATT);
-    renorm_attn_k<<<NB*4*NSL, 256, 0, stream>>>(ATT);
+    sm_renorm_k<<<16, 256, 0, stream>>>(ATT);
     slot_upd_k<<<MS, 256, 0, stream>>>(ATT, VB, UPD);
-    GEMMM(UPD, 0, oWo, sa_bo, 0, UPDP, 0, MS, DIM, 256, 0, 0, 1);
+    gemm_mfma<<<dim3(8, 4, 1), 256, 0, stream>>>(
+        UPD, 0, 0, nullptr, nullptr, 0, WTS, oWo, sa_bo, 0, UPDP, 0,
+        MS, DIM, 256, 0, 0, 1, 0, nullptr, nullptr, FLAG);
     gemm_mfma_duo<<<dim3(24, 4, 2), 256, 0, stream>>>(
-        UPDP, SLOTS, 0, WTS, oGih, oGhh, gru_bih, gru_bhh, GX, GH, 0, MS, 1536, DIM, FLAG);
+        UPDP, SLOTS, 0, 0, nullptr, nullptr,
+        WTS, oGih, oGhh, gru_bih, gru_bhh, GX, GH, 0, MS, 1536, DIM, FLAG);
     gru_k<<<CDIV(NB*NSL*DIM, 256), 256, 0, stream>>>(GX, GH, SLOTS);
-    ln512_k<<<MS, 256, 0, stream>>>(SLOTS, sa_ln_ff_g, sa_ln_ff_b, SLNB, FLAG);
-    GEMMM(SLNB, 1, oMlp1, sa_mlp_b1, 0, HIDSB, 1, MS, DIM, DIM, 1, 0, 1);
-    GEMMM(HIDSB, 1, oMlp2, sa_mlp_b2, 0, SLOTS, 0, MS, DIM, DIM, 0, 1, 1);
+    gemm_mfma<<<dim3(8, 4, 1), 256, 0, stream>>>(
+        SLOTS, 0, 1, sa_ln_ff_g, sa_ln_ff_b, 0, WTS, oMlp1, sa_mlp_b1, 0, HIDSB, 1,
+        MS, DIM, DIM, 1, 0, 1, 0, nullptr, nullptr, FLAG);
+    gemm_mfma<<<dim3(8, 4, 1), 256, 0, stream>>>(
+        HIDSB, 1, 0, nullptr, nullptr, 0, WTS, oMlp2, sa_mlp_b2, 0, SLOTS, 0,
+        MS, DIM, DIM, 0, 1, 1, 0, nullptr, nullptr, FLAG);
   }
 
   s2c_k<<<MS, 256, 0, stream>>>(SLOTS, s2c_w, s2c_b, SC, FLAG);
   build_coords_k<<<CDIV(NB*NT, 256), 256, 0, stream>>>(SC, CRD);
   relpos_table_k<<<961, 128, 0, stream>>>(rp_w1, rp_b1, rp_w2, rp_b2, rp_w3, rp_b3, TAB, FLAG);
   bias_fill_k<<<CDIV(NB*NH*HWT*HWT, 256), 256, 0, stream>>>(TAB, BIAS);
-  {
-    unsigned short* H1 = HBB;
-    unsigned short* H2 = HBB + (size_t)PCH * 128;
-    for (int c = 0; c < 2; ++c) {
-      int pb = c * PCH;
-      rp_l1_k<<<CDIV(PCH*128, 256), 256, 0, stream>>>(CRD, rp_w1, rp_b1, H1, pb, PCH, FLAG);
-      GEMMM(H1, 1, oRp2, rp_b2, 0, H2, 1, PCH, 128, 128, 3, 0, 1);
-      rp_l3_k<<<CDIV(PCH,32), 256, 0, stream>>>(H2, rp_w3, rp_b3, BIAS, pb, PCH, FLAG);
-    }
-  }
+  gemm_rp_k<<<CDIV(NB*RPP, 64), 256, 0, stream>>>(
+      CRD, rp_w1, rp_b1, WTS, oRp2, rp_b2, rp_w3, rp_b3, BIAS, FLAG);
 
   build_x_k<<<CDIV(NB*NT*DIM, 256), 256, 0, stream>>>(SLOTS, TOK, X);
   for (int l = 0; l < 6; ++l) {
     size_t lw = (size_t)l * 512 * 512;
-    rms512_k<<<MROW, 256, 0, stream>>>(X, attn_g, l * DIM, HBB, FLAG);
     gemm_mfma_tri<<<dim3(8, 20, 3), 256, 0, stream>>>(
-        HBB, 1, WTS, oWq + lw, oWk + lw, oWv + lw, QHB, KHB, VHB, 1, MROW, DIM, DIM, FLAG);
+        X, 0, 2, attn_g, l * DIM,
+        WTS, oWq + lw, oWk + lw, oWv + lw, QHB, KHB, VHB, 1, MROW, DIM, DIM, FLAG);
     attn_fused_k<<<dim3(10, NB*NH), 256, 0, stream>>>(QHB, KHB, VHB, BIAS, OBB);
-    GEMMM(OBB, 1, oWol + lw, (const void*)nullptr, 0, X, 0, MROW, DIM, DIM, 0, 1, 2);
-    rms512_k<<<MROW, 256, 0, stream>>>(X, ff_g, l * DIM, HBB, FLAG);
-    GEMMM(HBB, 1, oFf1 + (size_t)l * 512 * 2048, ff_b1, l * FF, FFHB, 1, MROW, FF, DIM, 2, 0, 1);
-    GEMMM(FFHB, 1, oFf2 + (size_t)l * 2048 * 512, ff_b2, l * DIM, X, 0, MROW, DIM, FF, 0, 1, 4);
-  }
-
-  rms512_k<<<MROW, 256, 0, stream>>>(X, final_g, 0, HBB, FLAG);
-  hipMemsetAsync(OUTT, 0, (size_t)NB * NT * DIM * sizeof(float), stream);
-  GEMMM(HBB, 1, oPred, pred_b, 0, OUTT, 0, MROW, DIM, DIM, 0, 0, 2);
-  write_out_k<<<CDIV(NB*HWT*DIM, 256), 256, 0, stream>>>(OUTT, d_out, FLAG);
-
-#undef GEMMM
-}
+    gemm_mfma<<<dim3(8, 20, 2), 256, 0, stream>>>(
+        OBB, 1, 0, nullptr, nullptr, 0, WTS, oWol + lw, (const void*)nullptr, 0, X, 0,
+        MROW, DIM, DIM, 0, 1, 2, 0, nullptr, nullptr, FLAG);
+    gemm_mfma<<<dim3(32, 20, 1), 256, 0, stream>>>(
+        X, 0, 2, ff_g, nullptr, l * DIM, WTS, oFf1 + (size_t)l * 512 * 2048, ff_b1, l * FF,
+        FFHB, 1, MROW, FF, DIM, 2, 0, 1, 0, nullptr, nullptr, FLAG);
+    gemm_mfma<<<dim3(8, 20, 4), 256, 0, stream>>>(
+        FFHB, 1, 0, nullptr, nullptr, 0, WTS, oFf2 + (size_t)l * 2048 * 512, ff_b2, l * DIM,
+        X, 0, MROW, DIM, FF, 0, 1, 4, 0, nullptr, nullptr, FLAG);
+  }
+
+  gemm_mfma<<<dim3(8, 20, 1), 256, 0, stream>>>(
+      X, 0, 2, final_g, nullptr, 0, WTS, oPred, pred_b, 0, d_out, 0,
+      MROW, DIM, DIM, 0, 0, 1, 1, nullptr, nullptr, FLAG);
+}
```

Result: slower. 1.474 ms (+25.7%).
